# Performance work log

Hardware: AMD Instinct MI355X
Metric: run time of the kernel (lower is better)

## Reference

```python
import jax, jax.numpy as jnp
import numpy as np

ALPHA = 0.2  # leakyrelu negative slope
NEG_INF = -1.0e12


def setup_inputs() -> dict:
    key = jax.random.key(0)
    k1, k2, k3, k4, k5 = jax.random.split(key, 5)
    B, N, C_in, C_out = 8, 2048, 256, 256
    inp = jax.random.normal(k1, (B, N, C_in), dtype=jnp.float32)
    adj = jax.random.randint(k2, (N, N), 0, 2, dtype=jnp.int32)
    # xavier_uniform with gain=1.414 for (C_in, C_out)
    limit = 1.414 * np.sqrt(6.0 / (C_in + C_out))
    W1 = jax.random.uniform(k3, (C_in, C_out), jnp.float32, -limit, limit)
    W2 = jax.random.uniform(k4, (C_in, C_out), jnp.float32, -limit, limit)
    W3 = jax.random.uniform(k5, (C_in, C_out), jnp.float32, -limit, limit)
    return {"inp": inp, "adj": adj, "W1": W1, "W2": W2, "W3": W3}


def reference(inp, adj, W1, W2, W3):
    # inp: [B,N,Cin], adj: [N,N], W*: [Cin,Cout]
    h1 = jnp.einsum('bnc,cd->bnd', inp, W1)  # [B,N,Cout] queries
    h2 = jnp.einsum('bnc,cd->bnd', inp, W2)  # [B,N,Cout] keys
    h3 = jnp.einsum('bnc,cd->bnd', inp, W3)  # [B,N,Cout] values
    e = jnp.einsum('bnd,bmd->bnm', h1, h2)   # [B,N,N] scores
    e = jax.nn.leaky_relu(e, ALPHA)
    e = jnp.where(adj[None, :, :] > 0, e, NEG_INF)
    attention = jax.nn.softmax(e, axis=-1)   # dropout p=0 / eval mode -> identity
    h_prime = jnp.einsum('bnm,bmd->bnd', attention, h3)
    return jax.nn.relu(h_prime)  # concat=True
```

## Files before the change

### kernel.cpp

```cpp
#include <hip/hip_runtime.h>

typedef __bf16 bf16_t;
typedef __bf16 bf16x4 __attribute__((ext_vector_type(4)));
typedef __bf16 bf16x8 __attribute__((ext_vector_type(8)));
typedef float floatx4 __attribute__((ext_vector_type(4)));
typedef signed char i8_t;
typedef int intx4 __attribute__((ext_vector_type(4)));

__device__ inline void split_hl(float v, bf16_t& hi, bf16_t& lo) {
    hi = (bf16_t)v;
    lo = (bf16_t)(v - (float)hi);
}

__global__ void adjbits_kernel(const int* __restrict__ adj, unsigned* __restrict__ bits) {
    int id = blockIdx.x * 256 + threadIdx.x;
    const int* p = adj + (size_t)id * 32;
    unsigned w = 0;
#pragma unroll
    for (int j = 0; j < 32; j += 4) {
        int4 v = *(const int4*)(p + j);
        w |= (v.x > 0 ? 1u : 0u) << j;
        w |= (v.y > 0 ? 1u : 0u) << (j + 1);
        w |= (v.z > 0 ? 1u : 0u) << (j + 2);
        w |= (v.w > 0 ? 1u : 0u) << (j + 3);
    }
    bits[id] = w;
}

__global__ void wtrans_kernel(const float* __restrict__ W1,
                              const float* __restrict__ W2,
                              const float* __restrict__ W3,
                              bf16_t* __restrict__ Wthi, bf16_t* __restrict__ Wtlo) {
    __shared__ float T[64 * 68];
    const int zi = blockIdx.z;
    const float* W = (zi == 0) ? W1 : ((zi == 1) ? W2 : W3);
    bf16_t* ohi = Wthi + zi * 256 * 256;
    bf16_t* olo = Wtlo + zi * 256 * 256;
    const int c0 = blockIdx.x * 64, d0 = blockIdx.y * 64;
    const int tid = threadIdx.x;
#pragma unroll
    for (int i = 0; i < 4; i++) {
        int idx = i * 256 + tid;
        int r = idx >> 4, c4 = (idx & 15) * 4;
        floatx4 v = *(const floatx4*)(W + (c0 + r) * 256 + d0 + c4);
        *(floatx4*)(&T[r * 68 + c4]) = v;
    }
    __syncthreads();
#pragma unroll
    for (int i = 0; i < 4; i++) {
        int idx = i * 256 + tid;
        int rd = idx & 63, cc4 = (idx >> 6) * 4;
        bf16x4 vh, vl;
#pragma unroll
        for (int ii = 0; ii < 4; ii++) {
            float v = T[(cc4 + ii) * 68 + rd];
            bf16_t h, l; split_hl(v, h, l);
            vh[ii] = h; vl[ii] = l;
        }
        *(bf16x4*)(ohi + (d0 + rd) * 256 + c0 + cc4) = vh;
        *(bf16x4*)(olo + (d0 + rd) * 256 + c0 + cc4) = vl;
    }
}

__global__ __launch_bounds__(256) void proj_kernel(
    const float* __restrict__ X,
    const bf16_t* __restrict__ Wthi, const bf16_t* __restrict__ Wtlo,
    i8_t* __restrict__ Q8h, i8_t* __restrict__ Q8l, float* __restrict__ sqv,
    i8_t* __restrict__ K8h, i8_t* __restrict__ K8l, float* __restrict__ skv,
    bf16_t* __restrict__ H3t) {
    __shared__ bf16_t Xh[64 * 40], Xl[64 * 40];
    __shared__ bf16_t Wh[256 * 40], Wl[256 * 40];
    const int z = blockIdx.y;
    const int row0 = blockIdx.x * 64;
    const int tid = threadIdx.x;
    const int w = tid >> 6, lane = tid & 63;
    const int m = lane & 15, q = lane >> 4;
    const bf16_t* Wzh = Wthi + z * 256 * 256;
    const bf16_t* Wzl = Wtlo + z * 256 * 256;

    floatx4 acc[16];
#pragma unroll
    for (int i = 0; i < 16; i++) acc[i] = (floatx4){0.f, 0.f, 0.f, 0.f};

    for (int c0 = 0; c0 < 256; c0 += 32) {
#pragma unroll
        for (int i = 0; i < 2; i++) {
            int idx = i * 256 + tid;
            int r = idx >> 3, c4 = (idx & 7) * 4;
            floatx4 v = *(const floatx4*)(X + (size_t)(row0 + r) * 256 + c0 + c4);
            bf16x4 vh, vl;
#pragma unroll
            for (int ii = 0; ii < 4; ii++) {
                bf16_t h, l; split_hl(v[ii], h, l);
                vh[ii] = h; vl[ii] = l;
            }
            *(bf16x4*)(&Xh[r * 40 + c4]) = vh;
            *(bf16x4*)(&Xl[r * 40 + c4]) = vl;
        }
#pragma unroll
        for (int i = 0; i < 4; i++) {
            int idx = i * 256 + tid;
            int d = idx >> 2, c8 = (idx & 3) * 8;
            *(bf16x8*)(&Wh[d * 40 + c8]) = *(const bf16x8*)(Wzh + d * 256 + c0 + c8);
            *(bf16x8*)(&Wl[d * 40 + c8]) = *(const bf16x8*)(Wzl + d * 256 + c0 + c8);
        }
        __syncthreads();
        bf16x8 ah = *(const bf16x8*)(&Xh[(w * 16 + m) * 40 + q * 8]);
        bf16x8 al = *(const bf16x8*)(&Xl[(w * 16 + m) * 40 + q * 8]);
#pragma unroll
        for (int nt = 0; nt < 16; nt++) {
            bf16x8 bh = *(const bf16x8*)(&Wh[(nt * 16 + m) * 40 + q * 8]);
            bf16x8 bl = *(const bf16x8*)(&Wl[(nt * 16 + m) * 40 + q * 8]);
            acc[nt] = __builtin_amdgcn_mfma_f32_16x16x32_bf16(ah, bh, acc[nt], 0, 0, 0);
            acc[nt] = __builtin_amdgcn_mfma_f32_16x16x32_bf16(ah, bl, acc[nt], 0, 0, 0);
            acc[nt] = __builtin_amdgcn_mfma_f32_16x16x32_bf16(al, bh, acc[nt], 0, 0, 0);
        }
        __syncthreads();
    }
    const int rbase = row0 + w * 16 + q * 4;
    if (z < 2) {
        i8_t* Dh = (z == 0) ? Q8h : K8h;
        i8_t* Dl = (z == 0) ? Q8l : K8l;
        float* sv = (z == 0) ? sqv : skv;
        float am[4] = {0.f, 0.f, 0.f, 0.f};
#pragma unroll
        for (int nt = 0; nt < 16; nt++)
#pragma unroll
            for (int r = 0; r < 4; r++) am[r] = fmaxf(am[r], fabsf(acc[nt][r]));
#pragma unroll
        for (int off = 1; off < 16; off <<= 1)
#pragma unroll
            for (int r = 0; r < 4; r++)
                am[r] = fmaxf(am[r], __shfl_xor(am[r], off, 64));
        float sc[4], inv[4];
#pragma unroll
        for (int r = 0; r < 4; r++) {
            sc[r]  = (am[r] > 0.f) ? am[r] * (1.f / 127.f) : 1.f;
            inv[r] = (am[r] > 0.f) ? 127.f / am[r] : 0.f;
        }
#pragma unroll
        for (int nt = 0; nt < 16; nt++)
#pragma unroll
            for (int r = 0; r < 4; r++) {
                float vq = acc[nt][r] * inv[r];
                float qh = rintf(vq);
                float ql = fminf(fmaxf(rintf((vq - qh) * 256.f), -127.f), 127.f);
                int offo = (rbase + r) * 256 + nt * 16 + m;
                Dh[offo] = (i8_t)(int)qh;
                Dl[offo] = (i8_t)(int)ql;
            }
        if (m == 0) {
#pragma unroll
            for (int r = 0; r < 4; r++) sv[rbase + r] = sc[r];
        }
    } else {
#pragma unroll
        for (int nt = 0; nt < 16; nt++)
#pragma unroll
            for (int r = 0; r < 4; r++) {
                int token = rbase + r;
                int b = token >> 11, n = token & 2047;
                H3t[(size_t)(b * 256 + nt * 16 + m) * 2048 + n] = (bf16_t)acc[nt][r];
            }
    }
}

#define K8SW(row, off) ((off) ^ (((row) & 7) << 4))
#define VSW(row, off)  ((off) ^ ((((row) >> 1) & 3) << 4))
__global__ __launch_bounds__(256, 2) void attn_kernel(
    const i8_t* __restrict__ Q8h, const i8_t* __restrict__ Q8l,
    const float* __restrict__ sqv,
    const i8_t* __restrict__ K8h, const i8_t* __restrict__ K8l,
    const float* __restrict__ skv,
    const bf16_t* __restrict__ H3t, const unsigned* __restrict__ adjbits,
    float* __restrict__ Opart, float* __restrict__ mpart, float* __restrict__ lpart,
    int klen) {
    __shared__ i8_t K8[2][32 * 256];
    __shared__ bf16_t Vl[256 * 32];
    __shared__ bf16_t Pl[4][16 * 32];

    const int nwg = (int)(gridDim.x * gridDim.y * gridDim.z);
    const int wgid = (int)(blockIdx.x + (blockIdx.y << 5) + (blockIdx.z << 8));
    const int nid = (wgid & 7) * (nwg >> 3) + (wgid >> 3);
    const int qb = nid & 31;
    const int b  = (nid >> 5) & 7;
    const int kz = nid >> 8;

    const int q0 = qb * 64;
    const int tid = threadIdx.x;
    const int w = tid >> 6, lane = tid & 63;
    const int m = lane & 15, q = lane >> 4;

    char* K8B0 = (char*)&K8[0][0];
    char* K8B1 = (char*)&K8[1][0];
    char* VlB  = (char*)&Vl[0];
    char* PlB  = (char*)&Pl[w][0];

    const i8_t* qrh = Q8h + (size_t)(b * 2048 + q0 + w * 16 + m) * 256;
    const i8_t* qrl = Q8l + (size_t)(b * 2048 + q0 + w * 16 + m) * 256;
    intx4 qh8[4], ql8[4];
#pragma unroll
    for (int ck = 0; ck < 4; ck++) {
        qh8[ck] = *(const intx4*)(qrh + ck * 64 + q * 16);
        ql8[ck] = *(const intx4*)(qrl + ck * 64 + q * 16);
    }
    float sq4[4];
#pragma unroll
    for (int r = 0; r < 4; r++) sq4[r] = sqv[b * 2048 + q0 + w * 16 + q * 4 + r];

    bf16x8 vones;
#pragma unroll
    for (int i = 0; i < 8; i++) vones[i] = (bf16_t)1.0f;

    float m_run[4];
#pragma unroll
    for (int r = 0; r < 4; r++) m_run[r] = -3.0e38f;
    floatx4 l_acc = (floatx4){0.f, 0.f, 0.f, 0.f};
    floatx4 o[16];
#pragma unroll
    for (int i = 0; i < 16; i++) o[i] = (floatx4){0.f, 0.f, 0.f, 0.f};

    const unsigned* bitrow[4];
#pragma unroll
    for (int r = 0; r < 4; r++)
        bitrow[r] = adjbits + (size_t)(q0 + w * 16 + q * 4 + r) * 64;

    intx4 rkh[2], rkl[2];
    bf16x8 rvv[4];
    float skt[2], skn[2];
    const int kbeg = kz * klen, kend = kbeg + klen;

#pragma unroll
    for (int i = 0; i < 2; i++) {
        int ci = i * 256 + tid;
        int kr = ci >> 4, cb = (ci & 15) * 16;
        rkh[i] = *(const intx4*)(K8h + (size_t)(b * 2048 + kbeg + kr) * 256 + cb);
        rkl[i] = *(const intx4*)(K8l + (size_t)(b * 2048 + kbeg + kr) * 256 + cb);
    }
#pragma unroll
    for (int i = 0; i < 4; i++) {
        int ci = i * 256 + tid;
        int d = ci >> 2, k8 = (ci & 3) * 8;
        rvv[i] = *(const bf16x8*)(H3t + (size_t)(b * 256 + d) * 2048 + kbeg + k8);
    }
    skt[0] = skv[b * 2048 + kbeg + m];
    skt[1] = skv[b * 2048 + kbeg + 16 + m];

    for (int k0 = kbeg; k0 < kend; k0 += 32) {
        __syncthreads();
#pragma unroll
        for (int i = 0; i < 2; i++) {
            int ci = i * 256 + tid;
            int kr = ci >> 4, cb = (ci & 15) * 16;
            *(intx4*)(K8B0 + K8SW(kr, kr * 256 + cb)) = rkh[i];
            *(intx4*)(K8B1 + K8SW(kr, kr * 256 + cb)) = rkl[i];
        }
#pragma unroll
        for (int i = 0; i < 4; i++) {
            int ci = i * 256 + tid;
            int d = ci >> 2, kb = (ci & 3) * 16;
            *(bf16x8*)(VlB + VSW(d, d * 64 + kb)) = rvv[i];
        }
        __syncthreads();
        if (k0 + 32 < kend) {
            int kn = k0 + 32;
#pragma unroll
            for (int i = 0; i < 2; i++) {
                int ci = i * 256 + tid;
                int kr = ci >> 4, cb = (ci & 15) * 16;
                rkh[i] = *(const intx4*)(K8h + (size_t)(b * 2048 + kn + kr) * 256 + cb);
                rkl[i] = *(const intx4*)(K8l + (size_t)(b * 2048 + kn + kr) * 256 + cb);
            }
#pragma unroll
            for (int i = 0; i < 4; i++) {
                int ci = i * 256 + tid;
                int d = ci >> 2, k8 = (ci & 3) * 8;
                rvv[i] = *(const bf16x8*)(H3t + (size_t)(b * 256 + d) * 2048 + kn + k8);
            }
            skn[0] = skv[b * 2048 + kn + m];
            skn[1] = skv[b * 2048 + kn + 16 + m];
        }

        float s[2][4];
#pragma unroll
        for (int t = 0; t < 2; t++) {
            intx4 ch = {0, 0, 0, 0}, cm = {0, 0, 0, 0};
            const int row = t * 16 + m;
#pragma unroll
            for (int ck = 0; ck < 4; ck++) {
                const int cb2 = ck * 64 + q * 16;
                intx4 kh = *(const intx4*)(K8B0 + K8SW(row, row * 256 + cb2));
                intx4 kl = *(const intx4*)(K8B1 + K8SW(row, row * 256 + cb2));
                ch = __builtin_amdgcn_mfma_i32_16x16x64_i8(qh8[ck], kh, ch, 0, 0, 0);
                cm = __builtin_amdgcn_mfma_i32_16x16x64_i8(qh8[ck], kl, cm, 0, 0, 0);
                cm = __builtin_amdgcn_mfma_i32_16x16x64_i8(ql8[ck], kh, cm, 0, 0, 0);
            }
#pragma unroll
            for (int r = 0; r < 4; r++)
                s[t][r] = fmaf((float)cm[r], 0.00390625f, (float)ch[r]) * (sq4[r] * skt[t]);
        }

        unsigned aw[4];
#pragma unroll
        for (int r = 0; r < 4; r++) aw[r] = bitrow[r][k0 >> 5];
        float p[2][4], tmax[4];
#pragma unroll
        for (int r = 0; r < 4; r++) tmax[r] = -3.0e38f;
#pragma unroll
        for (int t = 0; t < 2; t++)
#pragma unroll
            for (int r = 0; r < 4; r++) {
                float v = s[t][r];
                v = (v > 0.f) ? v : 0.2f * v;
                v = ((aw[r] >> (t * 16 + m)) & 1u) ? v : -1.0e12f;
                p[t][r] = v;
                tmax[r] = fmaxf(tmax[r], v);
            }
#pragma unroll
        for (int off = 1; off < 16; off <<= 1)
#pragma unroll
            for (int r = 0; r < 4; r++)
                tmax[r] = fmaxf(tmax[r], __shfl_xor(tmax[r], off, 64));

        int rise = 0;
        float mnew[4];
#pragma unroll
        for (int r = 0; r < 4; r++) {
            mnew[r] = fmaxf(m_run[r], tmax[r]);
            rise |= (mnew[r] > m_run[r]);
        }
        if (__any(rise)) {
#pragma unroll
            for (int r = 0; r < 4; r++) {
                float alpha = __expf(m_run[r] - mnew[r]);
                m_run[r] = mnew[r];
                l_acc[r] *= alpha;
#pragma unroll
                for (int nt = 0; nt < 16; nt++) o[nt][r] *= alpha;
            }
        }
#pragma unroll
        for (int t = 0; t < 2; t++)
#pragma unroll
            for (int r = 0; r < 4; r++)
                p[t][r] = __expf(p[t][r] - m_run[r]);

#pragma unroll
        for (int t = 0; t < 2; t++)
#pragma unroll
            for (int r = 0; r < 4; r++) {
                int row = q * 4 + r;
                *(bf16_t*)(PlB + VSW(row, row * 64 + (t * 16 + m) * 2)) = (bf16_t)p[t][r];
            }
        bf16x8 pf = *(const bf16x8*)(PlB + VSW(m, m * 64 + q * 16));

        l_acc = __builtin_amdgcn_mfma_f32_16x16x32_bf16(pf, vones, l_acc, 0, 0, 0);

#pragma unroll
        for (int nt = 0; nt < 16; nt++) {
            const int vr = nt * 16 + m;
            bf16x8 vf = *(const bf16x8*)(VlB + VSW(vr, vr * 64 + q * 16));
            o[nt] = __builtin_amdgcn_mfma_f32_16x16x32_bf16(pf, vf, o[nt], 0, 0, 0);
        }
        skt[0] = skn[0];
        skt[1] = skn[1];
    }

    const int rowg = kz * 16384 + b * 2048 + q0 + w * 16 + q * 4;
#pragma unroll
    for (int nt = 0; nt < 16; nt++)
#pragma unroll
        for (int r = 0; r < 4; r++)
            Opart[(size_t)(rowg + r) * 256 + nt * 16 + m] = o[nt][r];
    if (m == 0) {
#pragma unroll
        for (int r = 0; r < 4; r++) {
            mpart[rowg + r] = m_run[r];
            lpart[rowg + r] = l_acc[r];
        }
    }
}

__global__ __launch_bounds__(256) void merge_kernel(
    const float* __restrict__ Opart, const float* __restrict__ mpart,
    const float* __restrict__ lpart, float* __restrict__ out, int S) {
    int gid = blockIdx.x * 256 + threadIdx.x;
    int row = gid >> 6, c4 = (gid & 63) * 4;
    float M = -3.0e38f;
    for (int s = 0; s < S; s++) M = fmaxf(M, mpart[s * 16384 + row]);
    float denom = 0.f;
    float4 acc = make_float4(0.f, 0.f, 0.f, 0.f);
    for (int s = 0; s < S; s++) {
        float sc = __expf(mpart[s * 16384 + row] - M);
        denom += lpart[s * 16384 + row] * sc;
        float4 v = *(const float4*)(Opart + ((size_t)(s * 16384 + row)) * 256 + c4);
        acc.x += v.x * sc; acc.y += v.y * sc; acc.z += v.z * sc; acc.w += v.w * sc;
    }
    float inv = 1.f / denom;
    float4 r;
    r.x = fmaxf(acc.x * inv, 0.f);
    r.y = fmaxf(acc.y * inv, 0.f);
    r.z = fmaxf(acc.z * inv, 0.f);
    r.w = fmaxf(acc.w * inv, 0.f);
    *(float4*)(out + (size_t)row * 256 + c4) = r;
}

extern "C" void kernel_launch(void* const* d_in, const int* in_sizes, int n_in,
                              void* d_out, int out_size, void* d_ws, size_t ws_size,
                              hipStream_t stream) {
    const float* X   = (const float*)d_in[0];
    const int*   adj = (const int*)d_in[1];
    const float* W1  = (const float*)d_in[2];
    const float* W2  = (const float*)d_in[3];
    const float* W3  = (const float*)d_in[4];
    float* out = (float*)d_out;

    char* ws = (char*)d_ws;
    i8_t* Q8h = (i8_t*)(ws + ((size_t)0 << 20));
    i8_t* Q8l = (i8_t*)(ws + ((size_t)4 << 20));
    i8_t* K8h = (i8_t*)(ws + ((size_t)8 << 20));
    i8_t* K8l = (i8_t*)(ws + ((size_t)12 << 20));
    bf16_t* H3t = (bf16_t*)(ws + ((size_t)16 << 20));
    float* sqv = (float*)(ws + ((size_t)24 << 20));
    float* skv = (float*)(ws + ((size_t)24 << 20) + 65536);
    size_t wt0 = ((size_t)24 << 20) + 131072;
    bf16_t* Wthi = (bf16_t*)(ws + wt0);
    bf16_t* Wtlo = (bf16_t*)(ws + wt0 + 393216);
    float* mpart = (float*)(ws + wt0);
    float* lpart = (float*)(ws + wt0 + 131072);
    unsigned* adjb = (unsigned*)(ws + wt0 + 786432);
    size_t opart_off = wt0 + 786432 + 524288;
    const size_t need2 = opart_off + (size_t)2 * 16384 * 256 * 4;

    int S = (ws_size >= need2) ? 2 : 1;
    float* Opart = (S > 1) ? (float*)(ws + opart_off) : out;

    adjbits_kernel<<<512, 256, 0, stream>>>(adj, adjb);
    wtrans_kernel<<<dim3(4, 4, 3), 256, 0, stream>>>(W1, W2, W3, Wthi, Wtlo);
    proj_kernel<<<dim3(256, 3), 256, 0, stream>>>(X, Wthi, Wtlo,
                                                  Q8h, Q8l, sqv, K8h, K8l, skv, H3t);
    attn_kernel<<<dim3(32, 8, S), 256, 0, stream>>>(Q8h, Q8l, sqv, K8h, K8l, skv,
                                                    H3t, adjb, Opart, mpart, lpart,
                                                    2048 / S);
    merge_kernel<<<4096, 256, 0, stream>>>(Opart, mpart, lpart, out, S);
}
```

Measured before the change: 238.0 us.

## Split PV output by head-dim slices per wave, keep V in registers

Reassigns the P·V stage so each wave owns a 64-column slice of the output for all 64 query rows, instead of 16 rows by all 256 columns. Each wave loads its V fragments straight from global memory into registers, which drops the V shared-memory staging buffer and its stores and reads. The P tiles, rescale factors and rise flags of all four waves are now exchanged through shared memory behind an extra per-iteration barrier. The exchange and the conditional rescaling of the other waves' rows add synchronisation and some shared-memory traffic in exchange.

```diff
diff --git a/kernel.cpp b/kernel.cpp
--- a/kernel.cpp
+++ b/kernel.cpp
@@ -166,7 +166,7 @@
 }
 
 #define K8SW(row, off) ((off) ^ (((row) & 7) << 4))
-#define VSW(row, off)  ((off) ^ ((((row) >> 1) & 3) << 4))
+#define PSW(row, off)  ((off) ^ ((((row) >> 1) & 3) << 4))
 __global__ __launch_bounds__(256, 2) void attn_kernel(
     const i8_t* __restrict__ Q8h, const i8_t* __restrict__ Q8l,
     const float* __restrict__ sqv,
@@ -176,24 +176,24 @@
     float* __restrict__ Opart, float* __restrict__ mpart, float* __restrict__ lpart,
     int klen) {
     __shared__ i8_t K8[2][32 * 256];
-    __shared__ bf16_t Vl[256 * 32];
     __shared__ bf16_t Pl[4][16 * 32];
+    __shared__ __align__(16) float Al[4][16];
+    __shared__ __align__(16) int Fl[4];
 
     const int nwg = (int)(gridDim.x * gridDim.y * gridDim.z);
     const int wgid = (int)(blockIdx.x + (blockIdx.y << 5) + (blockIdx.z << 8));
     const int nid = (wgid & 7) * (nwg >> 3) + (wgid >> 3);
-    const int qb = nid & 31;
+    const int qblk = nid & 31;
     const int b  = (nid >> 5) & 7;
     const int kz = nid >> 8;
 
-    const int q0 = qb * 64;
+    const int q0 = qblk * 64;
     const int tid = threadIdx.x;
     const int w = tid >> 6, lane = tid & 63;
     const int m = lane & 15, q = lane >> 4;
 
     char* K8B0 = (char*)&K8[0][0];
     char* K8B1 = (char*)&K8[1][0];
-    char* VlB  = (char*)&Vl[0];
     char* PlB  = (char*)&Pl[w][0];
 
     const i8_t* qrh = Q8h + (size_t)(b * 2048 + q0 + w * 16 + m) * 256;
@@ -225,8 +225,10 @@
     for (int r = 0; r < 4; r++)
         bitrow[r] = adjbits + (size_t)(q0 + w * 16 + q * 4 + r) * 64;
 
+    const bf16_t* vbase = H3t + (size_t)(b * 256 + w * 64 + m) * 2048 + q * 8;
+
     intx4 rkh[2], rkl[2];
-    bf16x8 rvv[4];
+    bf16x8 vcur[4], vnxt[4];
     float skt[2], skn[2];
     const int kbeg = kz * klen, kend = kbeg + klen;
 
@@ -238,11 +240,8 @@
         rkl[i] = *(const intx4*)(K8l + (size_t)(b * 2048 + kbeg + kr) * 256 + cb);
     }
 #pragma unroll
-    for (int i = 0; i < 4; i++) {
-        int ci = i * 256 + tid;
-        int d = ci >> 2, k8 = (ci & 3) * 8;
-        rvv[i] = *(const bf16x8*)(H3t + (size_t)(b * 256 + d) * 2048 + kbeg + k8);
-    }
+    for (int dn = 0; dn < 4; dn++)
+        vcur[dn] = *(const bf16x8*)(vbase + (size_t)(dn * 16) * 2048 + kbeg);
     skt[0] = skv[b * 2048 + kbeg + m];
     skt[1] = skv[b * 2048 + kbeg + 16 + m];
 
@@ -255,12 +254,6 @@
             *(intx4*)(K8B0 + K8SW(kr, kr * 256 + cb)) = rkh[i];
             *(intx4*)(K8B1 + K8SW(kr, kr * 256 + cb)) = rkl[i];
         }
-#pragma unroll
-        for (int i = 0; i < 4; i++) {
-            int ci = i * 256 + tid;
-            int d = ci >> 2, kb = (ci & 3) * 16;
-            *(bf16x8*)(VlB + VSW(d, d * 64 + kb)) = rvv[i];
-        }
         __syncthreads();
         if (k0 + 32 < kend) {
             int kn = k0 + 32;
@@ -272,11 +265,8 @@
                 rkl[i] = *(const intx4*)(K8l + (size_t)(b * 2048 + kn + kr) * 256 + cb);
             }
 #pragma unroll
-            for (int i = 0; i < 4; i++) {
-                int ci = i * 256 + tid;
-                int d = ci >> 2, k8 = (ci & 3) * 8;
-                rvv[i] = *(const bf16x8*)(H3t + (size_t)(b * 256 + d) * 2048 + kn + k8);
-            }
+            for (int dn = 0; dn < 4; dn++)
+                vnxt[dn] = *(const bf16x8*)(vbase + (size_t)(dn * 16) * 2048 + kn);
             skn[0] = skv[b * 2048 + kn + m];
             skn[1] = skv[b * 2048 + kn + 16 + m];
         }
@@ -329,16 +319,19 @@
             mnew[r] = fmaxf(m_run[r], tmax[r]);
             rise |= (mnew[r] > m_run[r]);
         }
-        if (__any(rise)) {
+        const int rose = __any(rise);
+        if (rose) {
+            floatx4 a4;
 #pragma unroll
             for (int r = 0; r < 4; r++) {
                 float alpha = __expf(m_run[r] - mnew[r]);
                 m_run[r] = mnew[r];
                 l_acc[r] *= alpha;
-#pragma unroll
-                for (int nt = 0; nt < 16; nt++) o[nt][r] *= alpha;
-            }
-        }
+                a4[r] = alpha;
+            }
+            if (m == 0) *(floatx4*)(&Al[w][q * 4]) = a4;
+        }
+        if (lane == 0) Fl[w] = rose;
 #pragma unroll
         for (int t = 0; t < 2; t++)
 #pragma unroll
@@ -350,29 +343,55 @@
 #pragma unroll
             for (int r = 0; r < 4; r++) {
                 int row = q * 4 + r;
-                *(bf16_t*)(PlB + VSW(row, row * 64 + (t * 16 + m) * 2)) = (bf16_t)p[t][r];
-            }
-        bf16x8 pf = *(const bf16x8*)(PlB + VSW(m, m * 64 + q * 16));
-
-        l_acc = __builtin_amdgcn_mfma_f32_16x16x32_bf16(pf, vones, l_acc, 0, 0, 0);
-
-#pragma unroll
-        for (int nt = 0; nt < 16; nt++) {
-            const int vr = nt * 16 + m;
-            bf16x8 vf = *(const bf16x8*)(VlB + VSW(vr, vr * 64 + q * 16));
-            o[nt] = __builtin_amdgcn_mfma_f32_16x16x32_bf16(pf, vf, o[nt], 0, 0, 0);
-        }
+                *(bf16_t*)(PlB + PSW(row, row * 64 + (t * 16 + m) * 2)) = (bf16_t)p[t][r];
+            }
+        __syncthreads();
+
+        int4 fl4 = *(const int4*)(&Fl[0]);
+#pragma unroll
+        for (int qb = 0; qb < 4; qb++) {
+            int f = (qb == 0) ? fl4.x : (qb == 1) ? fl4.y : (qb == 2) ? fl4.z : fl4.w;
+            if (f) {
+                floatx4 a = *(const floatx4*)(&Al[qb][q * 4]);
+#pragma unroll
+                for (int dn = 0; dn < 4; dn++)
+#pragma unroll
+                    for (int r = 0; r < 4; r++) o[qb * 4 + dn][r] *= a[r];
+            }
+        }
+
+        bf16x8 pa[4];
+#pragma unroll
+        for (int qb = 0; qb < 4; qb++)
+            pa[qb] = *(const bf16x8*)((char*)&Pl[qb][0] + PSW(m, m * 64 + q * 16));
+#pragma unroll
+        for (int qb = 0; qb < 4; qb++)
+            if (qb == w)
+                l_acc = __builtin_amdgcn_mfma_f32_16x16x32_bf16(pa[qb], vones, l_acc, 0, 0, 0);
+#pragma unroll
+        for (int qb = 0; qb < 4; qb++)
+#pragma unroll
+            for (int dn = 0; dn < 4; dn++)
+                o[qb * 4 + dn] = __builtin_amdgcn_mfma_f32_16x16x32_bf16(
+                    pa[qb], vcur[dn], o[qb * 4 + dn], 0, 0, 0);
+
+#pragma unroll
+        for (int dn = 0; dn < 4; dn++) vcur[dn] = vnxt[dn];
         skt[0] = skn[0];
         skt[1] = skn[1];
     }
 
-    const int rowg = kz * 16384 + b * 2048 + q0 + w * 16 + q * 4;
-#pragma unroll
-    for (int nt = 0; nt < 16; nt++)
-#pragma unroll
-        for (int r = 0; r < 4; r++)
-            Opart[(size_t)(rowg + r) * 256 + nt * 16 + m] = o[nt][r];
+    const int rowbase = kz * 16384 + b * 2048 + q0;
+#pragma unroll
+    for (int qb = 0; qb < 4; qb++)
+#pragma unroll
+        for (int dn = 0; dn < 4; dn++)
+#pragma unroll
+            for (int r = 0; r < 4; r++)
+                Opart[(size_t)(rowbase + qb * 16 + q * 4 + r) * 256 + w * 64 + dn * 16 + m] =
+                    o[qb * 4 + dn][r];
     if (m == 0) {
+        const int rowg = rowbase + w * 16 + q * 4;
 #pragma unroll
         for (int r = 0; r < 4; r++) {
             mpart[rowg + r] = m_run[r];
```

After: 239.3 us. Within noise of the previous version (+0.6%).

## Double attention key tile to 64 and store split partials as bf16

Applied to the files above, without the earlier changes.

The flash-attention loop now processes 64 keys per iteration instead of 32. LDS K/V/P buffers, register prefetch staging and the adjacency-word reads grow to match, and each PV step issues two bf16 MFMAs per output tile. This halves the number of barrier-synchronized iterations and amortizes softmax bookkeeping over more keys, at the cost of more LDS (about 72KB per block) and more prefetch registers, which could hurt occupancy. Separately, the per-split partial output buffer is written and read as bf16 instead of fp32, cutting merge traffic but adding rounding error to the partial sums.

```diff
diff --git a/kernel.cpp b/kernel.cpp
--- a/kernel.cpp
+++ b/kernel.cpp
@@ -166,27 +166,27 @@
 }
 
 #define K8SW(row, off) ((off) ^ (((row) & 7) << 4))
-#define VSW(row, off)  ((off) ^ ((((row) >> 1) & 3) << 4))
+#define V2SW(row, off) ((off) ^ (((row) & 7) << 4))
 __global__ __launch_bounds__(256, 2) void attn_kernel(
     const i8_t* __restrict__ Q8h, const i8_t* __restrict__ Q8l,
     const float* __restrict__ sqv,
     const i8_t* __restrict__ K8h, const i8_t* __restrict__ K8l,
     const float* __restrict__ skv,
     const bf16_t* __restrict__ H3t, const unsigned* __restrict__ adjbits,
-    float* __restrict__ Opart, float* __restrict__ mpart, float* __restrict__ lpart,
+    bf16_t* __restrict__ Opart, float* __restrict__ mpart, float* __restrict__ lpart,
     int klen) {
-    __shared__ i8_t K8[2][32 * 256];
-    __shared__ bf16_t Vl[256 * 32];
-    __shared__ bf16_t Pl[4][16 * 32];
+    __shared__ i8_t K8[2][64 * 256];
+    __shared__ bf16_t Vl[256 * 64];
+    __shared__ bf16_t Pl[4][16 * 64];
 
     const int nwg = (int)(gridDim.x * gridDim.y * gridDim.z);
     const int wgid = (int)(blockIdx.x + (blockIdx.y << 5) + (blockIdx.z << 8));
     const int nid = (wgid & 7) * (nwg >> 3) + (wgid >> 3);
-    const int qb = nid & 31;
+    const int qblk = nid & 31;
     const int b  = (nid >> 5) & 7;
     const int kz = nid >> 8;
 
-    const int q0 = qb * 64;
+    const int q0 = qblk * 64;
     const int tid = threadIdx.x;
     const int w = tid >> 6, lane = tid & 63;
     const int m = lane & 15, q = lane >> 4;
@@ -225,65 +225,65 @@
     for (int r = 0; r < 4; r++)
         bitrow[r] = adjbits + (size_t)(q0 + w * 16 + q * 4 + r) * 64;
 
-    intx4 rkh[2], rkl[2];
-    bf16x8 rvv[4];
-    float skt[2], skn[2];
+    intx4 rkh[4], rkl[4];
+    bf16x8 rvv[8];
+    float skt[4], skn[4];
     const int kbeg = kz * klen, kend = kbeg + klen;
 
 #pragma unroll
-    for (int i = 0; i < 2; i++) {
+    for (int i = 0; i < 4; i++) {
         int ci = i * 256 + tid;
         int kr = ci >> 4, cb = (ci & 15) * 16;
         rkh[i] = *(const intx4*)(K8h + (size_t)(b * 2048 + kbeg + kr) * 256 + cb);
         rkl[i] = *(const intx4*)(K8l + (size_t)(b * 2048 + kbeg + kr) * 256 + cb);
     }
 #pragma unroll
-    for (int i = 0; i < 4; i++) {
+    for (int i = 0; i < 8; i++) {
         int ci = i * 256 + tid;
-        int d = ci >> 2, k8 = (ci & 3) * 8;
+        int d = ci >> 3, k8 = (ci & 7) * 8;
         rvv[i] = *(const bf16x8*)(H3t + (size_t)(b * 256 + d) * 2048 + kbeg + k8);
     }
-    skt[0] = skv[b * 2048 + kbeg + m];
-    skt[1] = skv[b * 2048 + kbeg + 16 + m];
-
-    for (int k0 = kbeg; k0 < kend; k0 += 32) {
+#pragma unroll
+    for (int t = 0; t < 4; t++) skt[t] = skv[b * 2048 + kbeg + t * 16 + m];
+
+    for (int k0 = kbeg; k0 < kend; k0 += 64) {
         __syncthreads();
 #pragma unroll
-        for (int i = 0; i < 2; i++) {
+        for (int i = 0; i < 4; i++) {
             int ci = i * 256 + tid;
             int kr = ci >> 4, cb = (ci & 15) * 16;
             *(intx4*)(K8B0 + K8SW(kr, kr * 256 + cb)) = rkh[i];
             *(intx4*)(K8B1 + K8SW(kr, kr * 256 + cb)) = rkl[i];
         }
 #pragma unroll
-        for (int i = 0; i < 4; i++) {
+        for (int i = 0; i < 8; i++) {
             int ci = i * 256 + tid;
-            int d = ci >> 2, kb = (ci & 3) * 16;
-            *(bf16x8*)(VlB + VSW(d, d * 64 + kb)) = rvv[i];
+            int d = ci >> 3, kb = (ci & 7) * 16;
+            *(bf16x8*)(VlB + V2SW(d, d * 128 + kb)) = rvv[i];
         }
         __syncthreads();
-        if (k0 + 32 < kend) {
-            int kn = k0 + 32;
-#pragma unroll
-            for (int i = 0; i < 2; i++) {
+        if (k0 + 64 < kend) {
+            int kn = k0 + 64;
+#pragma unroll
+            for (int i = 0; i < 4; i++) {
                 int ci = i * 256 + tid;
                 int kr = ci >> 4, cb = (ci & 15) * 16;
                 rkh[i] = *(const intx4*)(K8h + (size_t)(b * 2048 + kn + kr) * 256 + cb);
                 rkl[i] = *(const intx4*)(K8l + (size_t)(b * 2048 + kn + kr) * 256 + cb);
             }
 #pragma unroll
-            for (int i = 0; i < 4; i++) {
+            for (int i = 0; i < 8; i++) {
                 int ci = i * 256 + tid;
-                int d = ci >> 2, k8 = (ci & 3) * 8;
+                int d = ci >> 3, k8 = (ci & 7) * 8;
                 rvv[i] = *(const bf16x8*)(H3t + (size_t)(b * 256 + d) * 2048 + kn + k8);
             }
-            skn[0] = skv[b * 2048 + kn + m];
-            skn[1] = skv[b * 2048 + kn + 16 + m];
-        }
-
-        float s[2][4];
-#pragma unroll
-        for (int t = 0; t < 2; t++) {
+#pragma unroll
+            for (int t = 0; t < 4; t++) skn[t] = skv[b * 2048 + kn + t * 16 + m];
+        }
+
+        float s[4][4];
+#pragma unroll
+        for (int t = 0; t < 4; t++) {
             intx4 ch = {0, 0, 0, 0}, cm = {0, 0, 0, 0};
             const int row = t * 16 + m;
 #pragma unroll
@@ -300,19 +300,24 @@
                 s[t][r] = fmaf((float)cm[r], 0.00390625f, (float)ch[r]) * (sq4[r] * skt[t]);
         }
 
-        unsigned aw[4];
-#pragma unroll
-        for (int r = 0; r < 4; r++) aw[r] = bitrow[r][k0 >> 5];
-        float p[2][4], tmax[4];
+        unsigned aw0[4], aw1[4];
+#pragma unroll
+        for (int r = 0; r < 4; r++) {
+            aw0[r] = bitrow[r][k0 >> 5];
+            aw1[r] = bitrow[r][(k0 >> 5) + 1];
+        }
+        float p[4][4], tmax[4];
 #pragma unroll
         for (int r = 0; r < 4; r++) tmax[r] = -3.0e38f;
 #pragma unroll
-        for (int t = 0; t < 2; t++)
+        for (int t = 0; t < 4; t++)
 #pragma unroll
             for (int r = 0; r < 4; r++) {
                 float v = s[t][r];
                 v = (v > 0.f) ? v : 0.2f * v;
-                v = ((aw[r] >> (t * 16 + m)) & 1u) ? v : -1.0e12f;
+                unsigned bit = (t < 2) ? ((aw0[r] >> (t * 16 + m)) & 1u)
+                                       : ((aw1[r] >> ((t - 2) * 16 + m)) & 1u);
+                v = bit ? v : -1.0e12f;
                 p[t][r] = v;
                 tmax[r] = fmaxf(tmax[r], v);
             }
@@ -340,30 +345,34 @@
             }
         }
 #pragma unroll
-        for (int t = 0; t < 2; t++)
+        for (int t = 0; t < 4; t++)
 #pragma unroll
             for (int r = 0; r < 4; r++)
                 p[t][r] = __expf(p[t][r] - m_run[r]);
 
 #pragma unroll
-        for (int t = 0; t < 2; t++)
+        for (int t = 0; t < 4; t++)
 #pragma unroll
             for (int r = 0; r < 4; r++) {
                 int row = q * 4 + r;
-                *(bf16_t*)(PlB + VSW(row, row * 64 + (t * 16 + m) * 2)) = (bf16_t)p[t][r];
-            }
-        bf16x8 pf = *(const bf16x8*)(PlB + VSW(m, m * 64 + q * 16));
-
-        l_acc = __builtin_amdgcn_mfma_f32_16x16x32_bf16(pf, vones, l_acc, 0, 0, 0);
+                *(bf16_t*)(PlB + V2SW(row, row * 128 + (t * 16 + m) * 2)) = (bf16_t)p[t][r];
+            }
+        bf16x8 pf0 = *(const bf16x8*)(PlB + V2SW(m, m * 128 + q * 16));
+        bf16x8 pf1 = *(const bf16x8*)(PlB + V2SW(m, m * 128 + 64 + q * 16));
+
+        l_acc = __builtin_amdgcn_mfma_f32_16x16x32_bf16(pf0, vones, l_acc, 0, 0, 0);
+        l_acc = __builtin_amdgcn_mfma_f32_16x16x32_bf16(pf1, vones, l_acc, 0, 0, 0);
 
 #pragma unroll
         for (int nt = 0; nt < 16; nt++) {
             const int vr = nt * 16 + m;
-            bf16x8 vf = *(const bf16x8*)(VlB + VSW(vr, vr * 64 + q * 16));
-            o[nt] = __builtin_amdgcn_mfma_f32_16x16x32_bf16(pf, vf, o[nt], 0, 0, 0);
-        }
-        skt[0] = skn[0];
-        skt[1] = skn[1];
+            bf16x8 vf0 = *(const bf16x8*)(VlB + V2SW(vr, vr * 128 + q * 16));
+            bf16x8 vf1 = *(const bf16x8*)(VlB + V2SW(vr, vr * 128 + 64 + q * 16));
+            o[nt] = __builtin_amdgcn_mfma_f32_16x16x32_bf16(pf0, vf0, o[nt], 0, 0, 0);
+            o[nt] = __builtin_amdgcn_mfma_f32_16x16x32_bf16(pf1, vf1, o[nt], 0, 0, 0);
+        }
+#pragma unroll
+        for (int t = 0; t < 4; t++) skt[t] = skn[t];
     }
 
     const int rowg = kz * 16384 + b * 2048 + q0 + w * 16 + q * 4;
@@ -371,7 +380,7 @@
     for (int nt = 0; nt < 16; nt++)
 #pragma unroll
         for (int r = 0; r < 4; r++)
-            Opart[(size_t)(rowg + r) * 256 + nt * 16 + m] = o[nt][r];
+            Opart[(size_t)(rowg + r) * 256 + nt * 16 + m] = (bf16_t)o[nt][r];
     if (m == 0) {
 #pragma unroll
         for (int r = 0; r < 4; r++) {
@@ -382,7 +391,7 @@
 }
 
 __global__ __launch_bounds__(256) void merge_kernel(
-    const float* __restrict__ Opart, const float* __restrict__ mpart,
+    const bf16_t* __restrict__ Opart, const float* __restrict__ mpart,
     const float* __restrict__ lpart, float* __restrict__ out, int S) {
     int gid = blockIdx.x * 256 + threadIdx.x;
     int row = gid >> 6, c4 = (gid & 63) * 4;
@@ -393,8 +402,9 @@
     for (int s = 0; s < S; s++) {
         float sc = __expf(mpart[s * 16384 + row] - M);
         denom += lpart[s * 16384 + row] * sc;
-        float4 v = *(const float4*)(Opart + ((size_t)(s * 16384 + row)) * 256 + c4);
-        acc.x += v.x * sc; acc.y += v.y * sc; acc.z += v.z * sc; acc.w += v.w * sc;
+        bf16x4 v = *(const bf16x4*)(Opart + ((size_t)(s * 16384 + row)) * 256 + c4);
+        acc.x += (float)v[0] * sc; acc.y += (float)v[1] * sc;
+        acc.z += (float)v[2] * sc; acc.w += (float)v[3] * sc;
     }
     float inv = 1.f / denom;
     float4 r;
@@ -430,10 +440,10 @@
     float* lpart = (float*)(ws + wt0 + 131072);
     unsigned* adjb = (unsigned*)(ws + wt0 + 786432);
     size_t opart_off = wt0 + 786432 + 524288;
-    const size_t need2 = opart_off + (size_t)2 * 16384 * 256 * 4;
+    const size_t need2 = opart_off + (size_t)2 * 16384 * 256 * 2;
 
     int S = (ws_size >= need2) ? 2 : 1;
-    float* Opart = (S > 1) ? (float*)(ws + opart_off) : out;
+    bf16_t* Opart = (bf16_t*)(ws + opart_off);
 
     adjbits_kernel<<<512, 256, 0, stream>>>(adj, adjb);
     wtrans_kernel<<<dim3(4, 4, 3), 256, 0, stream>>>(W1, W2, W3, Wthi, Wtlo);
```

Result: slower. 489.1 us (+105.5%).
